# Kernel optimization log

Hardware: AMD Instinct MI355X
Metric: run time of the kernel (lower is better)

The kernel has to match this reference:

```python
import jax, jax.numpy as jnp
import numpy as np

B, S, E = 16, 1024, 512
D = 2 * E            # dim of concatenated embeddings, input to QKV and MLP
H1, H2 = 2048, 1024  # hidden_dims
SCALE = float(1.0 / np.sqrt(E))  # code scales by embedding_dim**0.5 (the init arg, not D)


def setup_inputs() -> dict:
    key = jax.random.key(0)
    k = jax.random.split(key, 12)

    def lin_w(kk, fan_in, fan_out):
        return jax.random.normal(kk, (fan_in, fan_out), jnp.float32) * float(1.0 / np.sqrt(fan_in))

    return {
        "emb1": jax.random.normal(k[0], (B, S, E), jnp.float32),
        "emb2": jax.random.normal(k[1], (B, S, E), jnp.float32),
        # query-row masks; all ones (a 0 would -inf an entire softmax row -> NaN)
        "mask1": jnp.ones((B, S // 2), jnp.int32),
        "mask2": jnp.ones((B, S // 2), jnp.int32),
        "Wq": lin_w(k[2], D, D), "bq": jnp.zeros((D,), jnp.float32),
        "Wk": lin_w(k[3], D, D), "bk": jnp.zeros((D,), jnp.float32),
        "Wv": lin_w(k[4], D, D), "bv": jnp.zeros((D,), jnp.float32),
        "W1": lin_w(k[5], D, H1), "b1": jnp.zeros((H1,), jnp.float32),
        "W2": lin_w(k[6], H1, H2), "b2": jnp.zeros((H2,), jnp.float32),
        "W3": lin_w(k[7], H2, 1), "b3": jnp.zeros((1,), jnp.float32),
    }


def reference(emb1, emb2, mask1, mask2, Wq, bq, Wk, bk, Wv, bv, W1, b1, W2, b2, W3, b3):
    x = jnp.concatenate([emb1, emb2], axis=-1)        # [B, S, D]
    mask = jnp.concatenate([mask1, mask2], axis=-1)   # [B, S] (query-row mask)

    # QKV self-attention with query-only mask
    Q = x @ Wq + bq
    K = x @ Wk + bk
    V = x @ Wv + bv
    scores = jnp.einsum("bqd,bkd->bqk", Q, K) * SCALE  # [B, S, S]
    scores = jnp.where(mask[:, :, None] == 0, -jnp.inf, scores)
    attn = jax.nn.softmax(scores, axis=-1)
    attended = jnp.einsum("bqk,bkd->bqd", attn, V)     # [B, S, D]

    # MLP head (Dropout is identity in eval mode)
    h = jax.nn.relu(attended @ W1 + b1)
    h = jax.nn.relu(h @ W2 + b2)
    logits = h @ W3 + b3                               # [B, S, 1]
    return jax.nn.sigmoid(logits)
```

## Files before the change

### kernel.cpp

```cpp
#include <hip/hip_runtime.h>
#include <math.h>

#define DEV __device__ __forceinline__

typedef unsigned short u16;
typedef unsigned int   u32;
typedef __bf16 bf16x8 __attribute__((ext_vector_type(8)));
typedef float  f32x4  __attribute__((ext_vector_type(4)));
typedef u16    u16x8  __attribute__((ext_vector_type(8)));
typedef u16    u16x4  __attribute__((ext_vector_type(4)));

DEV u16 f2b(float f) {
  u32 u = __builtin_bit_cast(u32, f);
  u = (u + 0x7FFFu + ((u >> 16) & 1u)) >> 16;
  return (u16)u;
}
DEV float b2f(u16 h) { u32 u = (u32)h << 16; return __builtin_bit_cast(float, u); }

DEV void gl_lds16(const u16* g, u16* l) {
  __builtin_amdgcn_global_load_lds((const __attribute__((address_space(1))) void*)g,
                                   (__attribute__((address_space(3))) void*)l, 16, 0, 0);
}

DEV float wred_max(float v) {
#pragma unroll
  for (int o = 32; o > 0; o >>= 1) v = fmaxf(v, __shfl_xor(v, o, 64));
  return v;
}
DEV float wred_sum(float v) {
#pragma unroll
  for (int o = 32; o > 0; o >>= 1) v += __shfl_xor(v, o, 64);
  return v;
}

__global__ __launch_bounds__(256) void concat_convert(
    const float* __restrict__ e1, const float* __restrict__ e2, u16* __restrict__ xb) {
  const size_t idx = ((size_t)blockIdx.x * 256 + threadIdx.x) * 8;
  const int d = (int)(idx & 1023);
  const size_t row = idx >> 10;
  const float* s = (d < 512) ? (e1 + row * 512 + d) : (e2 + row * 512 + (d - 512));
  f32x4 a = *(const f32x4*)s;
  f32x4 b = *(const f32x4*)(s + 4);
  u16x8 o;
  o[0]=f2b(a[0]); o[1]=f2b(a[1]); o[2]=f2b(a[2]); o[3]=f2b(a[3]);
  o[4]=f2b(b[0]); o[5]=f2b(b[1]); o[6]=f2b(b[2]); o[7]=f2b(b[3]);
  *(u16x8*)(xb + idx) = o;
}

__global__ __launch_bounds__(256) void transpose_w(
    const float* __restrict__ W, int ldi, u16* __restrict__ WT, int ldo) {
  __shared__ float tile[64][65];
  const int tx = threadIdx.x & 63, ty = threadIdx.x >> 6;
  const int r0 = blockIdx.y * 64, c0 = blockIdx.x * 64;
#pragma unroll
  for (int i = 0; i < 16; ++i)
    tile[ty + 4*i][tx] = W[(size_t)(r0 + ty + 4*i) * ldi + c0 + tx];
  __syncthreads();
#pragma unroll
  for (int i = 0; i < 16; ++i)
    WT[(size_t)(c0 + ty + 4*i) * ldo + r0 + tx] = f2b(tile[tx][ty + 4*i]);
}

__global__ __launch_bounds__(256) void transpose_v(
    const u16* __restrict__ in, int ldi, long long si,
    u16* __restrict__ out, int ldo, long long so) {
  __shared__ u16 tile[64][65];
  in  += (size_t)blockIdx.z * (size_t)si;
  out += (size_t)blockIdx.z * (size_t)so;
  const int tx = threadIdx.x & 63, ty = threadIdx.x >> 6;
  const int r0 = blockIdx.y * 64, c0 = blockIdx.x * 64;
#pragma unroll
  for (int i = 0; i < 16; ++i)
    tile[ty + 4*i][tx] = in[(size_t)(r0 + ty + 4*i) * ldi + c0 + tx];
  __syncthreads();
#pragma unroll
  for (int i = 0; i < 16; ++i)
    out[(size_t)(c0 + ty + 4*i) * ldo + r0 + tx] = tile[tx][ty + 4*i];
}

__global__ void concat_bias(const float* __restrict__ bq, const float* __restrict__ bk,
                            const float* __restrict__ bv, float* __restrict__ o) {
  int i = blockIdx.x * 256 + threadIdx.x;
  o[i] = (i < 1024) ? bq[i] : (i < 2048 ? bk[i - 1024] : bv[i - 2048]);
}

template<int F32OUT, int RELU>
__global__ __launch_bounds__(512, 2) void gemm256(
    const u16* __restrict__ A, int lda, long long sA,
    const u16* __restrict__ B, int ldb, long long sB,
    void* __restrict__ C, int ldc, long long sC,
    const float* __restrict__ bias, float scale, int K, int swz_gy) {
  __shared__ __align__(16) u16 lds[4][2][8192];

  const int t  = threadIdx.x;
  const int ln = t & 63, wv = t >> 6;

  int bx, by;
  if (gridDim.z == 1) {
    const int flat = blockIdx.y * gridDim.x + blockIdx.x;
    const int cpx  = (gridDim.x * gridDim.y) >> 3;
    const int L    = (flat & 7) * cpx + (flat >> 3);
    bx = L / swz_gy; by = L % swz_gy;
  } else { bx = blockIdx.x; by = blockIdx.y; }
  const int m0 = by * 256, n0 = bx * 256;
  const size_t bz = blockIdx.z;
  A += bz * (size_t)sA; B += bz * (size_t)sB;

  const int srow = t >> 2;
  const int sgr  = (t & 3) ^ ((t >> 3) & 3);
  const u16* gA = A + (size_t)(m0 + srow) * lda + sgr * 8;
  const u16* gB = B + (size_t)(n0 + srow) * ldb + sgr * 8;
  const size_t a128 = (size_t)128 * lda, b128 = (size_t)128 * ldb;
  const int ldst = wv * 512;

  const int l15 = ln & 15, lhi = ln >> 4;
  const int wm = (wv >> 2) * 128, wn = (wv & 3) * 64;

  int offA[8], offB[4];
#pragma unroll
  for (int i = 0; i < 8; ++i) {
    const int r = wm + i * 16 + l15;
    offA[i] = r * 32 + ((lhi ^ ((r >> 1) & 3)) << 3);
  }
#pragma unroll
  for (int j = 0; j < 4; ++j) {
    const int r = wn + j * 16 + l15;
    offB[j] = r * 32 + ((lhi ^ ((r >> 1) & 3)) << 3);
  }

  f32x4 acc[8][4] = {};
  const int KT = K >> 5;

#pragma unroll
  for (int pt = 0; pt < 3; ++pt) {
    const u16* _ga = gA + (size_t)pt * 32;
    const u16* _gb = gB + (size_t)pt * 32;
    u16* _la = &lds[pt][0][ldst];
    u16* _lb = &lds[pt][1][ldst];
    gl_lds16(_ga, _la); gl_lds16(_ga + a128, _la + 4096);
    gl_lds16(_gb, _lb); gl_lds16(_gb + b128, _lb + 4096);
  }
  asm volatile("s_waitcnt vmcnt(8)" ::: "memory");
  __builtin_amdgcn_sched_barrier(0);
  __builtin_amdgcn_s_barrier();

  for (int kt = 0; kt < KT; ++kt) {
    const u16* Abuf = &lds[kt & 3][0][0];
    const u16* Bbuf = &lds[kt & 3][1][0];
    const int  nt   = kt + 3;

    bf16x8 af[8];
#pragma unroll
    for (int i = 0; i < 8; ++i) af[i] = *(const bf16x8*)&Abuf[offA[i]];
    bf16x8 bf0 = *(const bf16x8*)&Bbuf[offB[0]];
    bf16x8 bf1 = *(const bf16x8*)&Bbuf[offB[1]];
    if (nt < KT) {
      const u16* _ga = gA + (size_t)nt * 32;
      u16* _la = &lds[nt & 3][0][ldst];
      gl_lds16(_ga, _la); gl_lds16(_ga + a128, _la + 4096);
    }
    __builtin_amdgcn_s_barrier();
    __builtin_amdgcn_s_setprio(1);
#pragma unroll
    for (int i = 0; i < 8; ++i) {
      acc[i][0] = __builtin_amdgcn_mfma_f32_16x16x32_bf16(af[i], bf0, acc[i][0], 0, 0, 0);
      acc[i][1] = __builtin_amdgcn_mfma_f32_16x16x32_bf16(af[i], bf1, acc[i][1], 0, 0, 0);
    }
    __builtin_amdgcn_s_setprio(0);
    __builtin_amdgcn_s_barrier();

    bf16x8 bf2 = *(const bf16x8*)&Bbuf[offB[2]];
    bf16x8 bf3 = *(const bf16x8*)&Bbuf[offB[3]];
    if (nt < KT) {
      const u16* _gb = gB + (size_t)nt * 32;
      u16* _lb = &lds[nt & 3][1][ldst];
      gl_lds16(_gb, _lb); gl_lds16(_gb + b128, _lb + 4096);
    }
    __builtin_amdgcn_s_barrier();
    __builtin_amdgcn_s_setprio(1);
#pragma unroll
    for (int i = 0; i < 8; ++i) {
      acc[i][2] = __builtin_amdgcn_mfma_f32_16x16x32_bf16(af[i], bf2, acc[i][2], 0, 0, 0);
      acc[i][3] = __builtin_amdgcn_mfma_f32_16x16x32_bf16(af[i], bf3, acc[i][3], 0, 0, 0);
    }
    __builtin_amdgcn_s_setprio(0);

    if (kt < KT - 3)       { asm volatile("s_waitcnt vmcnt(8)" ::: "memory"); }
    else if (kt == KT - 3) { asm volatile("s_waitcnt vmcnt(4)" ::: "memory"); }
    else if (kt == KT - 2) { asm volatile("s_waitcnt vmcnt(0)" ::: "memory"); }
    __builtin_amdgcn_sched_barrier(0);
    __builtin_amdgcn_s_barrier();
  }

  const size_t cb = bz * (size_t)sC;
#pragma unroll
  for (int i = 0; i < 8; ++i) {
    const int rg = m0 + wm + i * 16 + lhi * 4;
#pragma unroll
    for (int j = 0; j < 4; ++j) {
      const int cg = n0 + wn + j * 16 + l15;
      const float bsv = bias ? bias[cg] : 0.f;
#pragma unroll
      for (int r = 0; r < 4; ++r) {
        float v = acc[i][j][r] * scale + bsv;
        if (RELU) v = fmaxf(v, 0.f);
        if (F32OUT) ((float*)C)[cb + (size_t)(rg + r) * ldc + cg] = v;
        else        ((u16*)C)[cb + (size_t)(rg + r) * ldc + cg] = f2b(v);
      }
    }
  }
}

__global__ __launch_bounds__(256) void softmax_mask(
    const float* __restrict__ sc, const int* __restrict__ m1,
    const int* __restrict__ m2, u16* __restrict__ attn) {
  __shared__ float red[8];
  const int row = blockIdx.x;
  const int b = row >> 10, q = row & 1023;
  const int mk = (q < 512) ? m1[b * 512 + q] : m2[b * 512 + q - 512];
  f32x4 v = ((const f32x4*)(sc + (size_t)row * 1024))[threadIdx.x];
  if (mk == 0) { v[0] = v[1] = v[2] = v[3] = -INFINITY; }
  float mx = fmaxf(fmaxf(v[0], v[1]), fmaxf(v[2], v[3]));
  mx = wred_max(mx);
  const int ln = threadIdx.x & 63, wv = threadIdx.x >> 6;
  if (ln == 0) red[wv] = mx;
  __syncthreads();
  mx = fmaxf(fmaxf(red[0], red[1]), fmaxf(red[2], red[3]));
  float e0 = __expf(v[0] - mx), e1 = __expf(v[1] - mx);
  float e2 = __expf(v[2] - mx), e3 = __expf(v[3] - mx);
  float s = wred_sum(e0 + e1 + e2 + e3);
  if (ln == 0) red[4 + wv] = s;
  __syncthreads();
  const float inv = 1.f / (red[4] + red[5] + red[6] + red[7]);
  u16x4 o; o[0] = f2b(e0 * inv); o[1] = f2b(e1 * inv); o[2] = f2b(e2 * inv); o[3] = f2b(e3 * inv);
  *(u16x4*)(attn + (size_t)row * 1024 + threadIdx.x * 4) = o;
}

__global__ __launch_bounds__(256) void logits_sigmoid(
    const u16* __restrict__ h2, const float* __restrict__ W3,
    const float* __restrict__ b3, float* __restrict__ out) {
  const int wid = (blockIdx.x * 256 + threadIdx.x) >> 6;
  const int ln = threadIdx.x & 63;
  const u16* r = h2 + (size_t)wid * 1024 + ln * 16;
  u16x8 v0 = *(const u16x8*)r;
  u16x8 v1 = *(const u16x8*)(r + 8);
  const float* w = W3 + ln * 16;
  float s = 0.f;
#pragma unroll
  for (int i = 0; i < 8; ++i) s += b2f(v0[i]) * w[i];
#pragma unroll
  for (int i = 0; i < 8; ++i) s += b2f(v1[i]) * w[8 + i];
#pragma unroll
  for (int o = 32; o > 0; o >>= 1) s += __shfl_down(s, o, 64);
  if (ln == 0) out[wid] = 1.f / (1.f + __expf(-(s + b3[0])));
}

extern "C" void kernel_launch(void* const* d_in, const int* in_sizes, int n_in,
                              void* d_out, int out_size, void* d_ws, size_t ws_size,
                              hipStream_t stream) {
  (void)in_sizes; (void)n_in; (void)out_size; (void)ws_size;
  const float* emb1 = (const float*)d_in[0];
  const float* emb2 = (const float*)d_in[1];
  const int*   mask1 = (const int*)d_in[2];
  const int*   mask2 = (const int*)d_in[3];
  const float* Wq = (const float*)d_in[4];  const float* bq = (const float*)d_in[5];
  const float* Wk = (const float*)d_in[6];  const float* bk = (const float*)d_in[7];
  const float* Wv = (const float*)d_in[8];  const float* bv = (const float*)d_in[9];
  const float* W1 = (const float*)d_in[10]; const float* b1 = (const float*)d_in[11];
  const float* W2 = (const float*)d_in[12]; const float* b2 = (const float*)d_in[13];
  const float* W3 = (const float*)d_in[14]; const float* b3 = (const float*)d_in[15];

  char* ws = (char*)d_ws;
  u16*  QKV   = (u16*)(ws + 0);
  u16*  VT    = (u16*)(ws + 100663296);
  u16*  XB    = (u16*)(ws + 134217728);
  u16*  WTQKV = (u16*)(ws + 167772160);
  u16*  W1T   = (u16*)(ws + 174063616);
  u16*  W2T   = (u16*)(ws + 178257920);
  float* SC   = (float*)(ws + 182452224);
  float* BF_  = (float*)(ws + 249561088);
  u16*  ATTN  = XB;
  u16*  ATT   = (u16*)(ws + 182452224);
  u16*  H1    = (u16*)(ws + 0);
  u16*  H2    = (u16*)(ws + 67108864);
  float* out  = (float*)d_out;

  const float SCALE = 0.04419417382415922f;

  concat_convert<<<8192, 256, 0, stream>>>(emb1, emb2, XB);
  transpose_w<<<dim3(16, 16), 256, 0, stream>>>(Wq, 1024, WTQKV, 1024);
  transpose_w<<<dim3(16, 16), 256, 0, stream>>>(Wk, 1024, WTQKV + 1024 * 1024, 1024);
  transpose_w<<<dim3(16, 16), 256, 0, stream>>>(Wv, 1024, WTQKV + 2048 * 1024, 1024);
  transpose_w<<<dim3(32, 16), 256, 0, stream>>>(W1, 2048, W1T, 1024);
  transpose_w<<<dim3(16, 32), 256, 0, stream>>>(W2, 1024, W2T, 2048);
  concat_bias<<<12, 256, 0, stream>>>(bq, bk, bv, BF_);

  gemm256<0, 0><<<dim3(12, 64, 1), 512, 0, stream>>>(
      XB, 1024, 0, WTQKV, 1024, 0, QKV, 3072, 0, BF_, 1.f, 1024, 64);
  transpose_v<<<dim3(16, 16, 16), 256, 0, stream>>>(
      QKV + 2048, 3072, 3145728LL, VT, 1024, 1048576LL);
  gemm256<1, 0><<<dim3(4, 4, 16), 512, 0, stream>>>(
      QKV, 3072, 3145728LL, QKV + 1024, 3072, 3145728LL,
      SC, 1024, 1048576LL, nullptr, SCALE, 1024, 4);
  softmax_mask<<<16384, 256, 0, stream>>>(SC, mask1, mask2, ATTN);
  gemm256<0, 0><<<dim3(4, 4, 16), 512, 0, stream>>>(
      ATTN, 1024, 1048576LL, VT, 1024, 1048576LL,
      ATT, 1024, 1048576LL, nullptr, 1.f, 1024, 4);
  gemm256<0, 1><<<dim3(8, 64, 1), 512, 0, stream>>>(
      ATT, 1024, 0, W1T, 1024, 0, H1, 2048, 0, b1, 1.f, 1024, 64);
  gemm256<0, 1><<<dim3(4, 64, 1), 512, 0, stream>>>(
      H1, 2048, 0, W2T, 2048, 0, H2, 1024, 0, b2, 1.f, 2048, 64);
  logits_sigmoid<<<4096, 256, 0, stream>>>(H2, W3, b3, out);
}
```

Baseline: 431.0 us.

## Compute V transposed directly via swapped GEMM, new tile swizzle, reorder MFMA loads

```diff
diff --git a/kernel.cpp b/kernel.cpp
--- a/kernel.cpp
+++ b/kernel.cpp
@@ -61,50 +61,44 @@
     WT[(size_t)(c0 + ty + 4*i) * ldo + r0 + tx] = f2b(tile[tx][ty + 4*i]);
 }
 
-__global__ __launch_bounds__(256) void transpose_v(
-    const u16* __restrict__ in, int ldi, long long si,
-    u16* __restrict__ out, int ldo, long long so) {
-  __shared__ u16 tile[64][65];
-  in  += (size_t)blockIdx.z * (size_t)si;
-  out += (size_t)blockIdx.z * (size_t)so;
-  const int tx = threadIdx.x & 63, ty = threadIdx.x >> 6;
-  const int r0 = blockIdx.y * 64, c0 = blockIdx.x * 64;
-#pragma unroll
-  for (int i = 0; i < 16; ++i)
-    tile[ty + 4*i][tx] = in[(size_t)(r0 + ty + 4*i) * ldi + c0 + tx];
-  __syncthreads();
-#pragma unroll
-  for (int i = 0; i < 16; ++i)
-    out[(size_t)(c0 + ty + 4*i) * ldo + r0 + tx] = tile[tx][ty + 4*i];
-}
-
 __global__ void concat_bias(const float* __restrict__ bq, const float* __restrict__ bk,
-                            const float* __restrict__ bv, float* __restrict__ o) {
+                            float* __restrict__ o) {
   int i = blockIdx.x * 256 + threadIdx.x;
-  o[i] = (i < 1024) ? bq[i] : (i < 2048 ? bk[i - 1024] : bv[i - 2048]);
-}
-
-template<int F32OUT, int RELU>
+  o[i] = (i < 1024) ? bq[i] : bk[i - 1024];
+}
+
+template<int F32OUT, int RELU, int RBIAS>
 __global__ __launch_bounds__(512, 2) void gemm256(
     const u16* __restrict__ A, int lda, long long sA,
     const u16* __restrict__ B, int ldb, long long sB,
     void* __restrict__ C, int ldc, long long sC,
-    const float* __restrict__ bias, float scale, int K, int swz_gy) {
+    const float* __restrict__ bias, float scale, int K) {
   __shared__ __align__(16) u16 lds[4][2][8192];
 
   const int t  = threadIdx.x;
   const int ln = t & 63, wv = t >> 6;
 
-  int bx, by;
-  if (gridDim.z == 1) {
-    const int flat = blockIdx.y * gridDim.x + blockIdx.x;
-    const int cpx  = (gridDim.x * gridDim.y) >> 3;
-    const int L    = (flat & 7) * cpx + (flat >> 3);
-    bx = L / swz_gy; by = L % swz_gy;
-  } else { bx = blockIdx.x; by = blockIdx.y; }
+  int bx, by, bz;
+  {
+    const int gx = gridDim.x, gy = gridDim.y, gz = gridDim.z;
+    const int nwg = gx * gy * gz;
+    const int F = (blockIdx.z * gy + blockIdx.y) * gx + blockIdx.x;
+    const int q = nwg >> 3;
+    const int L = (F & 7) * q + (F >> 3);
+    if (gz > 1) {
+      const int pb = gx * gy;
+      bz = L / pb; const int r = L - bz * pb;
+      by = r / gx; bx = r - by * gx;
+    } else {
+      bz = 0;
+      const int sh = ((gy & 7) == 0) ? 8 : 4;
+      const int sw = gx * sh;
+      const int sy = L / sw; const int r = L - sy * sw;
+      bx = r / sh; by = sy * sh + (r - bx * sh);
+    }
+  }
   const int m0 = by * 256, n0 = bx * 256;
-  const size_t bz = blockIdx.z;
-  A += bz * (size_t)sA; B += bz * (size_t)sB;
+  A += (size_t)bz * (size_t)sA; B += (size_t)bz * (size_t)sB;
 
   const int srow = t >> 2;
   const int sgr  = (t & 3) ^ ((t >> 3) & 3);
@@ -149,11 +143,14 @@
     const u16* Bbuf = &lds[kt & 3][1][0];
     const int  nt   = kt + 3;
 
-    bf16x8 af[8];
-#pragma unroll
-    for (int i = 0; i < 8; ++i) af[i] = *(const bf16x8*)&Abuf[offA[i]];
-    bf16x8 bf0 = *(const bf16x8*)&Bbuf[offB[0]];
-    bf16x8 bf1 = *(const bf16x8*)&Bbuf[offB[1]];
+    bf16x8 a0 = *(const bf16x8*)&Abuf[offA[0]];
+    bf16x8 a1 = *(const bf16x8*)&Abuf[offA[1]];
+    bf16x8 a2 = *(const bf16x8*)&Abuf[offA[2]];
+    bf16x8 a3 = *(const bf16x8*)&Abuf[offA[3]];
+    bf16x8 b0 = *(const bf16x8*)&Bbuf[offB[0]];
+    bf16x8 b1 = *(const bf16x8*)&Bbuf[offB[1]];
+    bf16x8 b2 = *(const bf16x8*)&Bbuf[offB[2]];
+    bf16x8 b3 = *(const bf16x8*)&Bbuf[offB[3]];
     if (nt < KT) {
       const u16* _ga = gA + (size_t)nt * 32;
       u16* _la = &lds[nt & 3][0][ldst];
@@ -161,16 +158,29 @@
     }
     __builtin_amdgcn_s_barrier();
     __builtin_amdgcn_s_setprio(1);
-#pragma unroll
-    for (int i = 0; i < 8; ++i) {
-      acc[i][0] = __builtin_amdgcn_mfma_f32_16x16x32_bf16(af[i], bf0, acc[i][0], 0, 0, 0);
-      acc[i][1] = __builtin_amdgcn_mfma_f32_16x16x32_bf16(af[i], bf1, acc[i][1], 0, 0, 0);
-    }
+    acc[0][0] = __builtin_amdgcn_mfma_f32_16x16x32_bf16(a0, b0, acc[0][0], 0, 0, 0);
+    acc[0][1] = __builtin_amdgcn_mfma_f32_16x16x32_bf16(a0, b1, acc[0][1], 0, 0, 0);
+    acc[0][2] = __builtin_amdgcn_mfma_f32_16x16x32_bf16(a0, b2, acc[0][2], 0, 0, 0);
+    acc[0][3] = __builtin_amdgcn_mfma_f32_16x16x32_bf16(a0, b3, acc[0][3], 0, 0, 0);
+    acc[1][0] = __builtin_amdgcn_mfma_f32_16x16x32_bf16(a1, b0, acc[1][0], 0, 0, 0);
+    acc[1][1] = __builtin_amdgcn_mfma_f32_16x16x32_bf16(a1, b1, acc[1][1], 0, 0, 0);
+    acc[1][2] = __builtin_amdgcn_mfma_f32_16x16x32_bf16(a1, b2, acc[1][2], 0, 0, 0);
+    acc[1][3] = __builtin_amdgcn_mfma_f32_16x16x32_bf16(a1, b3, acc[1][3], 0, 0, 0);
+    acc[2][0] = __builtin_amdgcn_mfma_f32_16x16x32_bf16(a2, b0, acc[2][0], 0, 0, 0);
+    acc[2][1] = __builtin_amdgcn_mfma_f32_16x16x32_bf16(a2, b1, acc[2][1], 0, 0, 0);
+    acc[2][2] = __builtin_amdgcn_mfma_f32_16x16x32_bf16(a2, b2, acc[2][2], 0, 0, 0);
+    acc[2][3] = __builtin_amdgcn_mfma_f32_16x16x32_bf16(a2, b3, acc[2][3], 0, 0, 0);
+    acc[3][0] = __builtin_amdgcn_mfma_f32_16x16x32_bf16(a3, b0, acc[3][0], 0, 0, 0);
+    acc[3][1] = __builtin_amdgcn_mfma_f32_16x16x32_bf16(a3, b1, acc[3][1], 0, 0, 0);
+    acc[3][2] = __builtin_amdgcn_mfma_f32_16x16x32_bf16(a3, b2, acc[3][2], 0, 0, 0);
+    acc[3][3] = __builtin_amdgcn_mfma_f32_16x16x32_bf16(a3, b3, acc[3][3], 0, 0, 0);
     __builtin_amdgcn_s_setprio(0);
     __builtin_amdgcn_s_barrier();
 
-    bf16x8 bf2 = *(const bf16x8*)&Bbuf[offB[2]];
-    bf16x8 bf3 = *(const bf16x8*)&Bbuf[offB[3]];
+    bf16x8 a4 = *(const bf16x8*)&Abuf[offA[4]];
+    bf16x8 a5 = *(const bf16x8*)&Abuf[offA[5]];
+    bf16x8 a6 = *(const bf16x8*)&Abuf[offA[6]];
+    bf16x8 a7 = *(const bf16x8*)&Abuf[offA[7]];
     if (nt < KT) {
       const u16* _gb = gB + (size_t)nt * 32;
       u16* _lb = &lds[nt & 3][1][ldst];
@@ -178,11 +188,22 @@
     }
     __builtin_amdgcn_s_barrier();
     __builtin_amdgcn_s_setprio(1);
-#pragma unroll
-    for (int i = 0; i < 8; ++i) {
-      acc[i][2] = __builtin_amdgcn_mfma_f32_16x16x32_bf16(af[i], bf2, acc[i][2], 0, 0, 0);
-      acc[i][3] = __builtin_amdgcn_mfma_f32_16x16x32_bf16(af[i], bf3, acc[i][3], 0, 0, 0);
-    }
+    acc[4][0] = __builtin_amdgcn_mfma_f32_16x16x32_bf16(a4, b0, acc[4][0], 0, 0, 0);
+    acc[4][1] = __builtin_amdgcn_mfma_f32_16x16x32_bf16(a4, b1, acc[4][1], 0, 0, 0);
+    acc[4][2] = __builtin_amdgcn_mfma_f32_16x16x32_bf16(a4, b2, acc[4][2], 0, 0, 0);
+    acc[4][3] = __builtin_amdgcn_mfma_f32_16x16x32_bf16(a4, b3, acc[4][3], 0, 0, 0);
+    acc[5][0] = __builtin_amdgcn_mfma_f32_16x16x32_bf16(a5, b0, acc[5][0], 0, 0, 0);
+    acc[5][1] = __builtin_amdgcn_mfma_f32_16x16x32_bf16(a5, b1, acc[5][1], 0, 0, 0);
+    acc[5][2] = __builtin_amdgcn_mfma_f32_16x16x32_bf16(a5, b2, acc[5][2], 0, 0, 0);
+    acc[5][3] = __builtin_amdgcn_mfma_f32_16x16x32_bf16(a5, b3, acc[5][3], 0, 0, 0);
+    acc[6][0] = __builtin_amdgcn_mfma_f32_16x16x32_bf16(a6, b0, acc[6][0], 0, 0, 0);
+    acc[6][1] = __builtin_amdgcn_mfma_f32_16x16x32_bf16(a6, b1, acc[6][1], 0, 0, 0);
+    acc[6][2] = __builtin_amdgcn_mfma_f32_16x16x32_bf16(a6, b2, acc[6][2], 0, 0, 0);
+    acc[6][3] = __builtin_amdgcn_mfma_f32_16x16x32_bf16(a6, b3, acc[6][3], 0, 0, 0);
+    acc[7][0] = __builtin_amdgcn_mfma_f32_16x16x32_bf16(a7, b0, acc[7][0], 0, 0, 0);
+    acc[7][1] = __builtin_amdgcn_mfma_f32_16x16x32_bf16(a7, b1, acc[7][1], 0, 0, 0);
+    acc[7][2] = __builtin_amdgcn_mfma_f32_16x16x32_bf16(a7, b2, acc[7][2], 0, 0, 0);
+    acc[7][3] = __builtin_amdgcn_mfma_f32_16x16x32_bf16(a7, b3, acc[7][3], 0, 0, 0);
     __builtin_amdgcn_s_setprio(0);
 
     if (kt < KT - 3)       { asm volatile("s_waitcnt vmcnt(8)" ::: "memory"); }
@@ -192,17 +213,17 @@
     __builtin_amdgcn_s_barrier();
   }
 
-  const size_t cb = bz * (size_t)sC;
+  const size_t cb = (size_t)bz * (size_t)sC;
 #pragma unroll
   for (int i = 0; i < 8; ++i) {
     const int rg = m0 + wm + i * 16 + lhi * 4;
 #pragma unroll
     for (int j = 0; j < 4; ++j) {
       const int cg = n0 + wn + j * 16 + l15;
-      const float bsv = bias ? bias[cg] : 0.f;
+      const float cbv = (!RBIAS && bias) ? bias[cg] : 0.f;
 #pragma unroll
       for (int r = 0; r < 4; ++r) {
-        float v = acc[i][j][r] * scale + bsv;
+        float v = acc[i][j][r] * scale + (RBIAS ? bias[rg + r] : cbv);
         if (RELU) v = fmaxf(v, 0.f);
         if (F32OUT) ((float*)C)[cb + (size_t)(rg + r) * ldc + cg] = v;
         else        ((u16*)C)[cb + (size_t)(rg + r) * ldc + cg] = f2b(v);
@@ -271,18 +292,18 @@
   const float* W3 = (const float*)d_in[14]; const float* b3 = (const float*)d_in[15];
 
   char* ws = (char*)d_ws;
-  u16*  QKV   = (u16*)(ws + 0);
+  u16*  XB    = (u16*)(ws + 0);
+  u16*  QK    = (u16*)(ws + 33554432);
   u16*  VT    = (u16*)(ws + 100663296);
-  u16*  XB    = (u16*)(ws + 134217728);
-  u16*  WTQKV = (u16*)(ws + 167772160);
-  u16*  W1T   = (u16*)(ws + 174063616);
-  u16*  W2T   = (u16*)(ws + 178257920);
-  float* SC   = (float*)(ws + 182452224);
-  float* BF_  = (float*)(ws + 249561088);
+  float* SC   = (float*)(ws + 134217728);
+  u16*  WTQKV = (u16*)(ws + 201326592);
+  u16*  W1T   = (u16*)(ws + 207618048);
+  u16*  W2T   = (u16*)(ws + 211812352);
+  float* BF_  = (float*)(ws + 216006656);
   u16*  ATTN  = XB;
-  u16*  ATT   = (u16*)(ws + 182452224);
-  u16*  H1    = (u16*)(ws + 0);
-  u16*  H2    = (u16*)(ws + 67108864);
+  u16*  ATT   = (u16*)(ws + 134217728);
+  u16*  H1    = QK;
+  u16*  H2    = VT;
   float* out  = (float*)d_out;
 
   const float SCALE = 0.04419417382415922f;
@@ -293,22 +314,22 @@
   transpose_w<<<dim3(16, 16), 256, 0, stream>>>(Wv, 1024, WTQKV + 2048 * 1024, 1024);
   transpose_w<<<dim3(32, 16), 256, 0, stream>>>(W1, 2048, W1T, 1024);
   transpose_w<<<dim3(16, 32), 256, 0, stream>>>(W2, 1024, W2T, 2048);
-  concat_bias<<<12, 256, 0, stream>>>(bq, bk, bv, BF_);
-
-  gemm256<0, 0><<<dim3(12, 64, 1), 512, 0, stream>>>(
-      XB, 1024, 0, WTQKV, 1024, 0, QKV, 3072, 0, BF_, 1.f, 1024, 64);
-  transpose_v<<<dim3(16, 16, 16), 256, 0, stream>>>(
-      QKV + 2048, 3072, 3145728LL, VT, 1024, 1048576LL);
-  gemm256<1, 0><<<dim3(4, 4, 16), 512, 0, stream>>>(
-      QKV, 3072, 3145728LL, QKV + 1024, 3072, 3145728LL,
-      SC, 1024, 1048576LL, nullptr, SCALE, 1024, 4);
+  concat_bias<<<8, 256, 0, stream>>>(bq, bk, BF_);
+
+  gemm256<0, 0, 0><<<dim3(8, 64, 1), 512, 0, stream>>>(
+      XB, 1024, 0, WTQKV, 1024, 0, QK, 2048, 0, BF_, 1.f, 1024);
+  gemm256<0, 0, 1><<<dim3(64, 4, 1), 512, 0, stream>>>(
+      WTQKV + 2048 * 1024, 1024, 0, XB, 1024, 0, VT, 16384, 0, bv, 1.f, 1024);
+  gemm256<1, 0, 0><<<dim3(4, 4, 16), 512, 0, stream>>>(
+      QK, 2048, 2097152LL, QK + 1024, 2048, 2097152LL,
+      SC, 1024, 1048576LL, nullptr, SCALE, 1024);
   softmax_mask<<<16384, 256, 0, stream>>>(SC, mask1, mask2, ATTN);
-  gemm256<0, 0><<<dim3(4, 4, 16), 512, 0, stream>>>(
-      ATTN, 1024, 1048576LL, VT, 1024, 1048576LL,
-      ATT, 1024, 1048576LL, nullptr, 1.f, 1024, 4);
-  gemm256<0, 1><<<dim3(8, 64, 1), 512, 0, stream>>>(
-      ATT, 1024, 0, W1T, 1024, 0, H1, 2048, 0, b1, 1.f, 1024, 64);
-  gemm256<0, 1><<<dim3(4, 64, 1), 512, 0, stream>>>(
-      H1, 2048, 0, W2T, 2048, 0, H2, 1024, 0, b2, 1.f, 2048, 64);
+  gemm256<0, 0, 0><<<dim3(4, 4, 16), 512, 0, stream>>>(
+      ATTN, 1024, 1048576LL, VT, 16384, 1024LL,
+      ATT, 1024, 1048576LL, nullptr, 1.f, 1024);
+  gemm256<0, 1, 0><<<dim3(8, 64, 1), 512, 0, stream>>>(
+      ATT, 1024, 0, W1T, 1024, 0, H1, 2048, 0, b1, 1.f, 1024);
+  gemm256<0, 1, 0><<<dim3(4, 64, 1), 512, 0, stream>>>(
+      H1, 2048, 0, W2T, 2048, 0, H2, 1024, 0, b2, 1.f, 2048);
   logits_sigmoid<<<4096, 256, 0, stream>>>(H2, W3, b3, out);
 }
```

Result: faster. 414.0 us (-3.9%).
